# Performance work log

Measured on AMD Instinct MI355X. Metric: run time of the kernel, lower is better.

## Reference

```python
import jax, jax.numpy as jnp
import numpy as np

B, T, E_A, E_B, E_ATT, N_HEAD = 2, 2048, 2048, 2048, 2048, 16
HS = E_ATT // N_HEAD  # 128
ROPE_BASE = 100000.0


def setup_inputs() -> dict:
    key = jax.random.key(0)
    ks = jax.random.split(key, 6)
    Ta = T // 2
    x_a = jax.random.normal(ks[0], (B, Ta, E_A), jnp.float32)
    x_b = jax.random.normal(ks[1], (B, T - Ta, E_B), jnp.float32)
    # alternating text/other tokens: even positions are stream-a
    mask_a = jnp.tile((jnp.arange(T) % 2 == 0)[None, :], (B, 1))
    # standard RoPE tables, full head_size (freqs duplicated), as litgpt/nanoGPT build them
    pos = jnp.arange(T, dtype=jnp.float32)
    inv_freq = 1.0 / (ROPE_BASE ** (jnp.arange(0, HS, 2, dtype=jnp.float32) / HS))
    freqs = pos[:, None] * inv_freq[None, :]           # [T, HS/2]
    emb = jnp.concatenate([freqs, freqs], axis=-1)      # [T, HS]
    cos, sin = jnp.cos(emb), jnp.sin(emb)
    s = 0.02
    Wqkv_a = jax.random.normal(ks[2], (E_A, 3 * E_ATT), jnp.float32) * s
    Wqkv_b = jax.random.normal(ks[3], (E_B, 3 * E_ATT), jnp.float32) * s
    Wproj_a = jax.random.normal(ks[4], (E_ATT, E_A), jnp.float32) * s
    Wproj_b = jax.random.normal(ks[5], (E_ATT, E_B), jnp.float32) * s
    return dict(x_a=x_a, x_b=x_b, cos=cos, sin=sin, mask_a=mask_a,
                Wqkv_a=Wqkv_a, Wqkv_b=Wqkv_b, Wproj_a=Wproj_a, Wproj_b=Wproj_b)


def _apply_rope(x, cos, sin):
    # x: [B, H, T, HS]; cos/sin: [T, HS] broadcast over leading dims
    x1 = x[..., : HS // 2]
    x2 = x[..., HS // 2:]
    rot = jnp.concatenate([-x2, x1], axis=-1)
    return (x * cos + rot * sin).astype(x.dtype)


def reference(x_a, x_b, cos, sin, mask_a, Wqkv_a, Wqkv_b, Wproj_a, Wproj_b):
    Bm, Tm = mask_a.shape
    Na = x_a.shape[0] * x_a.shape[1]  # static token counts per stream
    Nb = x_b.shape[0] * x_b.shape[1]
    C3 = Wqkv_a.shape[1]              # 3 * E_ATT
    # dual-stream QKV projections (bias=False)
    qkv_a = (x_a @ Wqkv_a).reshape(-1, C3)
    qkv_b = (x_b @ Wqkv_b).reshape(-1, C3)
    # interleave tokens back into the full [B, T] layout by mask scatter
    flat = mask_a.reshape(-1)
    idx_a = jnp.nonzero(flat, size=Na)[0]
    idx_b = jnp.nonzero(~flat, size=Nb)[0]
    kqv = jnp.zeros((Bm * Tm, C3), qkv_a.dtype).at[idx_a].set(qkv_a).at[idx_b].set(qkv_b)
    kqv = kqv.reshape(Bm, Tm, 3 * N_HEAD, HS).transpose(0, 2, 1, 3)  # [B, 3H, T, hs]
    q, k, v = kqv[:, :N_HEAD], kqv[:, N_HEAD:2 * N_HEAD], kqv[:, 2 * N_HEAD:]
    q = _apply_rope(q, cos, sin)
    k = _apply_rope(k, cos, sin)
    # causal SDPA (dropout_p = 0 at eval)
    scale = 1.0 / np.sqrt(HS).astype(np.float32)
    att = jnp.einsum('bhqd,bhkd->bhqk', q, k) * scale
    causal = jnp.tril(jnp.ones((Tm, Tm), bool))
    att = jnp.where(causal, att, -jnp.inf)
    att = jax.nn.softmax(att, axis=-1)
    y = jnp.einsum('bhqk,bhkd->bhqd', att, v)
    y = y.transpose(0, 2, 1, 3).reshape(Bm * Tm, N_HEAD * HS)
    # mask split + per-stream output projections
    y_a = y[idx_a] @ Wproj_a
    y_b = y[idx_b] @ Wproj_b
    return (y_a, y_b)
```

## Files before the change

kernel.cpp:

```cpp
#include <hip/hip_runtime.h>
#include <hip/hip_bf16.h>


typedef __attribute__((ext_vector_type(8))) short v8s;
typedef __attribute__((ext_vector_type(4))) float v4f;

#define GL2LDS(gptr, lptr)                                              \
  __builtin_amdgcn_global_load_lds(                                     \
      (const __attribute__((address_space(1))) void*)(gptr),            \
      (__attribute__((address_space(3))) void*)(lptr), 16, 0, 0)

__device__ __forceinline__ float b2f(unsigned short u) {
  return __uint_as_float(((unsigned int)u) << 16);
}
__device__ __forceinline__ unsigned short f2bf(float f) {
  unsigned int u = __float_as_uint(f);
  u += 0x7fffu + ((u >> 16) & 1u);
  return (unsigned short)(u >> 16);
}

__global__ __launch_bounds__(256) void f32_to_bf16_2(
    const float4* __restrict__ a, const float4* __restrict__ b,
    uint2* __restrict__ out, int n4each) {
  int i = blockIdx.x * 256 + threadIdx.x;
  if (i >= 2 * n4each) return;
  float4 v = (i < n4each) ? a[i] : b[i - n4each];
  uint2 o;
  o.x = (unsigned int)f2bf(v.x) | ((unsigned int)f2bf(v.y) << 16);
  o.y = (unsigned int)f2bf(v.z) | ((unsigned int)f2bf(v.w) << 16);
  out[i] = o;
}

__global__ __launch_bounds__(256) void transpose_f32_bf16(
    const float* __restrict__ in0, const float* __restrict__ in1,
    unsigned short* __restrict__ out0, unsigned short* __restrict__ out1,
    int R, int C) {
  const float* in = blockIdx.z ? in1 : in0;
  unsigned short* out = blockIdx.z ? out1 : out0;
  __shared__ unsigned short tile[64][65];
  const int bc = blockIdx.x * 64, br = blockIdx.y * 64;
  const int c  = threadIdx.x & 63;
  const int r0 = threadIdx.x >> 6;
  for (int r = r0; r < 64; r += 4)
    tile[r][c] = f2bf(in[(size_t)(br + r) * C + bc + c]);
  __syncthreads();
  for (int rr = r0; rr < 64; rr += 4)
    out[(size_t)(bc + rr) * R + br + c] = tile[c][rr];
}

template <int MODE>
__device__ __forceinline__ int amap(int r) {
  if constexpr (MODE == 0) return r;
  else return ((r >> 10) << 11) + ((r & 1023) << 1) + (MODE - 1);
}

template <int OMODE>
__global__ __launch_bounds__(256) void gemm_bt(
    const unsigned short* __restrict__ A, const unsigned short* __restrict__ BT,
    unsigned short* __restrict__ C, int M, int N, int K) {
  __shared__ __align__(16) unsigned short As[128 * 32];
  __shared__ __align__(16) unsigned short Bs[128 * 32];
  const int tid = threadIdx.x;
  const int w = tid >> 6, lane = tid & 63;
  const int m0 = blockIdx.x * 128, n0 = blockIdx.y * 128;
  const int wr = (w >> 1) * 64, wc = (w & 1) * 64;
  const int r = lane & 15, q = lane >> 4;

  const int cA  = w * 128 + lane;
  const int row = cA >> 2, kc = cA & 3;
  const unsigned short* gA0 = A  + (size_t)(m0 + row)      * K + kc * 8;
  const unsigned short* gA1 = A  + (size_t)(m0 + row + 16) * K + kc * 8;
  const unsigned short* gB0 = BT + (size_t)(n0 + row)      * K + kc * 8;
  const unsigned short* gB1 = BT + (size_t)(n0 + row + 16) * K + kc * 8;

  v4f acc[4][4] = {};

  for (int k0 = 0; k0 < K; k0 += 32) {
    GL2LDS(gA0 + k0, &As[w * 1024]);
    GL2LDS(gA1 + k0, &As[w * 1024 + 512]);
    GL2LDS(gB0 + k0, &Bs[w * 1024]);
    GL2LDS(gB1 + k0, &Bs[w * 1024 + 512]);
    __builtin_amdgcn_s_waitcnt(0);
    __syncthreads();

    v8s af[4], bf[4];
#pragma unroll
    for (int t = 0; t < 4; ++t) {
      af[t] = *(const v8s*)&As[(wr + t * 16 + r) * 32 + q * 8];
      bf[t] = *(const v8s*)&Bs[(wc + t * 16 + r) * 32 + q * 8];
    }
#pragma unroll
    for (int tm = 0; tm < 4; ++tm)
#pragma unroll
      for (int tn = 0; tn < 4; ++tn)
        acc[tm][tn] = __builtin_amdgcn_mfma_f32_16x16x32_bf16(
            af[tm], bf[tn], acc[tm][tn], 0, 0, 0);
    __builtin_amdgcn_s_waitcnt(0);
    __syncthreads();
  }

#pragma unroll
  for (int tm = 0; tm < 4; ++tm) {
    const int rowm = wr + tm * 16 + q * 4;
#pragma unroll
    for (int tn = 0; tn < 4; ++tn) {
      const int col = n0 + wc + tn * 16 + r;
#pragma unroll
      for (int p = 0; p < 4; ++p) {
        const int orow = amap<OMODE>(m0 + rowm + p);
        C[(size_t)orow * N + col] = f2bf(acc[tm][tn][p]);
      }
    }
  }
}

__global__ __launch_bounds__(256) void gemm_proj(
    const unsigned short* __restrict__ A, const unsigned short* __restrict__ BT0,
    const unsigned short* __restrict__ BT1, float* __restrict__ Cout,
    int M, int N, int K) {
  const int par = blockIdx.z;
  const unsigned short* BT = par ? BT1 : BT0;
  float* C = Cout + (size_t)par * M * N;
  __shared__ __align__(16) unsigned short As[128 * 32];
  __shared__ __align__(16) unsigned short Bs[128 * 32];
  const int tid = threadIdx.x;
  const int w = tid >> 6, lane = tid & 63;
  const int m0 = blockIdx.x * 128, n0 = blockIdx.y * 128;
  const int wr = (w >> 1) * 64, wc = (w & 1) * 64;
  const int r = lane & 15, q = lane >> 4;

  const int cA  = w * 128 + lane;
  const int row = cA >> 2, kc = cA & 3;
  const int ar0 = m0 + row, ar1 = m0 + row + 16;
  const int g0 = ((ar0 >> 10) << 11) + ((ar0 & 1023) << 1) + par;
  const int g1 = ((ar1 >> 10) << 11) + ((ar1 & 1023) << 1) + par;
  const unsigned short* gA0 = A  + (size_t)g0 * K + kc * 8;
  const unsigned short* gA1 = A  + (size_t)g1 * K + kc * 8;
  const unsigned short* gB0 = BT + (size_t)(n0 + row)      * K + kc * 8;
  const unsigned short* gB1 = BT + (size_t)(n0 + row + 16) * K + kc * 8;

  v4f acc[4][4] = {};

  for (int k0 = 0; k0 < K; k0 += 32) {
    GL2LDS(gA0 + k0, &As[w * 1024]);
    GL2LDS(gA1 + k0, &As[w * 1024 + 512]);
    GL2LDS(gB0 + k0, &Bs[w * 1024]);
    GL2LDS(gB1 + k0, &Bs[w * 1024 + 512]);
    __builtin_amdgcn_s_waitcnt(0);
    __syncthreads();

    v8s af[4], bf[4];
#pragma unroll
    for (int t = 0; t < 4; ++t) {
      af[t] = *(const v8s*)&As[(wr + t * 16 + r) * 32 + q * 8];
      bf[t] = *(const v8s*)&Bs[(wc + t * 16 + r) * 32 + q * 8];
    }
#pragma unroll
    for (int tm = 0; tm < 4; ++tm)
#pragma unroll
      for (int tn = 0; tn < 4; ++tn)
        acc[tm][tn] = __builtin_amdgcn_mfma_f32_16x16x32_bf16(
            af[tm], bf[tn], acc[tm][tn], 0, 0, 0);
    __builtin_amdgcn_s_waitcnt(0);
    __syncthreads();
  }

#pragma unroll
  for (int tm = 0; tm < 4; ++tm) {
    const int rowm = m0 + wr + tm * 16 + q * 4;
#pragma unroll
    for (int tn = 0; tn < 4; ++tn) {
      const int col = n0 + wc + tn * 16 + r;
#pragma unroll
      for (int p = 0; p < 4; ++p)
        C[(size_t)(rowm + p) * N + col] = acc[tm][tn][p];
    }
  }
}

__global__ __launch_bounds__(256) void scatter_rope(
    const unsigned short* __restrict__ qkv,
    const float* __restrict__ cosb, const float* __restrict__ sinb,
    unsigned short* __restrict__ Q, unsigned short* __restrict__ K) {
  const int token = blockIdx.x;
  const int b = token >> 11, t = token & 2047;
  const unsigned short* src = qkv + (size_t)token * 6144;
  for (int i = threadIdx.x; i < 2048; i += 256) {
    const int d = i & 127, h = i >> 7;
    const float cv = cosb[t * 128 + d];
    const float sv = sinb[t * 128 + d];
    const int   mate = (d < 64) ? i + 64 : i - 64;
    const float sgn  = (d < 64) ? -1.f : 1.f;
    const float qv = b2f(src[i]),        qm = b2f(src[mate]) * sgn;
    const float kv = b2f(src[2048 + i]), km = b2f(src[2048 + mate]) * sgn;
    const size_t off = ((size_t)(b * 16 + h) * 2048 + t) * 128 + d;
    Q[off] = f2bf(qv * cv + qm * sv);
    K[off] = f2bf(kv * cv + km * sv);
  }
}

__global__ __launch_bounds__(256) void transpose_v(
    const unsigned short* __restrict__ qkv, unsigned short* __restrict__ Vt) {
  __shared__ unsigned short tile[128][129];
  const int bh = blockIdx.x >> 4, tt = blockIdx.x & 15;
  const int b = bh >> 4, h = bh & 15;
  const int tid = threadIdx.x;
  const int d0 = tid & 127, t0 = tid >> 7;
#pragma unroll 4
  for (int i = 0; i < 64; ++i) {
    int tl = i * 2 + t0;
    tile[tl][d0] =
        qkv[((size_t)(b * 2048 + tt * 128 + tl)) * 6144 + 4096 + h * 128 + d0];
  }
  __syncthreads();
#pragma unroll 4
  for (int i = 0; i < 64; ++i) {
    int dd = i * 2 + t0;
    Vt[((size_t)(bh * 128 + dd)) * 2048 + tt * 128 + d0] = tile[d0][dd];
  }
}

#define SIG 0.1275174038536989f

__global__ __launch_bounds__(256, 2) void attn_flash(
    const unsigned short* __restrict__ Q, const unsigned short* __restrict__ K,
    const unsigned short* __restrict__ Vt, unsigned short* __restrict__ Y) {
  __shared__ __align__(16) unsigned short Ks[64 * 128];
  __shared__ __align__(16) unsigned short Vs[128 * 64];
  __shared__ __align__(16) unsigned short QP[64 * 128];

  const int bh = blockIdx.x >> 4, pr = blockIdx.x & 15;
  const int tid = threadIdx.x, w = tid >> 6, lane = tid & 63;
  const int r = lane & 15, q = lane >> 4;
  const int b = bh >> 4, h = bh & 15;
  const size_t kbase = (size_t)bh * 2048 * 128;
  const size_t vbase = (size_t)bh * 128 * 2048;

  for (int ph = 0; ph < 2; ++ph) {
    const int qt = ph ? pr : (31 - pr);

    const size_t qbase = ((size_t)bh * 2048 + qt * 64) * 128;
#pragma unroll
    for (int i = 0; i < 4; ++i) {
      const int rowl = w * 16 + i * 4 + q;
      const int g = r ^ (rowl & 15);
      GL2LDS(Q + qbase + (size_t)rowl * 128 + g * 8, &QP[(w * 16 + i * 4) * 128]);
    }
    __builtin_amdgcn_s_waitcnt(0);
    v8s qf[4];
#pragma unroll
    for (int ki = 0; ki < 4; ++ki) {
      const int rowl = w * 16 + r;
      const int c = (ki * 4 + q) ^ r;
      qf[ki] = *(const v8s*)&QP[rowl * 128 + c * 8];
    }
    __syncthreads();

    float mrun[4], lrun[4];
    v4f O[8] = {};
#pragma unroll
    for (int p = 0; p < 4; ++p) { mrun[p] = -3.0e38f; lrun[p] = 0.f; }

    const int nkt = qt + 1;
    for (int kt = 0; kt < nkt; ++kt) {
#pragma unroll
      for (int i = 0; i < 4; ++i) {
        const int key = w * 16 + i * 4 + q;
        const int g = r ^ (key & 15);
        GL2LDS(K + kbase + ((size_t)kt * 64 + key) * 128 + g * 8,
               &Ks[(w * 16 + i * 4) * 128]);
      }
      const int vrow = lane >> 3, pc = lane & 7;
#pragma unroll
      for (int i = 0; i < 4; ++i) {
        const int d = w * 32 + i * 8 + vrow;
        const int g = pc ^ (d & 7);
        GL2LDS(Vt + vbase + (size_t)d * 2048 + kt * 64 + g * 8,
               &Vs[(w * 32 + i * 8) * 64]);
      }
      __builtin_amdgcn_s_waitcnt(0);
      __syncthreads();

      v4f S[4] = {};
#pragma unroll
      for (int ki = 0; ki < 4; ++ki) {
        v8s kf[4];
#pragma unroll
        for (int tn = 0; tn < 4; ++tn) {
          const int key = tn * 16 + r;
          const int c = (ki * 4 + q) ^ r;
          kf[tn] = *(const v8s*)&Ks[key * 128 + c * 8];
        }
#pragma unroll
        for (int tn = 0; tn < 4; ++tn)
          S[tn] = __builtin_amdgcn_mfma_f32_16x16x32_bf16(
              qf[ki], kf[tn], S[tn], 0, 0, 0);
      }

      if (kt == qt) {
#pragma unroll
        for (int tn = 0; tn < 4; ++tn)
#pragma unroll
          for (int p = 0; p < 4; ++p) {
            const int tq = w * 16 + q * 4 + p;
            const int kg = tn * 16 + r;
            if (kg > tq) S[tn][p] = -3.0e38f;
          }
      }

#pragma unroll
      for (int p = 0; p < 4; ++p) {
        float mx = fmaxf(fmaxf(S[0][p], S[1][p]), fmaxf(S[2][p], S[3][p]));
#pragma unroll
        for (int o = 1; o < 16; o <<= 1) mx = fmaxf(mx, __shfl_xor(mx, o, 64));
        const float mnew = fmaxf(mrun[p], mx);
        const float alpha = exp2f((mrun[p] - mnew) * SIG);
        mrun[p] = mnew;
        float sum = 0.f;
#pragma unroll
        for (int tn = 0; tn < 4; ++tn) {
          const float pv = exp2f((S[tn][p] - mnew) * SIG);
          S[tn][p] = pv;
          sum += pv;
        }
#pragma unroll
        for (int o = 1; o < 16; o <<= 1) sum += __shfl_xor(sum, o, 64);
        lrun[p] = lrun[p] * alpha + sum;
#pragma unroll
        for (int tn = 0; tn < 8; ++tn) O[tn][p] *= alpha;
      }

#pragma unroll
      for (int tn = 0; tn < 4; ++tn)
#pragma unroll
        for (int p = 0; p < 4; ++p) {
          const int m = w * 16 + q * 4 + p;
          QP[m * 72 + tn * 16 + r] = f2bf(S[tn][p]);
        }

#pragma unroll
      for (int ki = 0; ki < 2; ++ki) {
        v8s pf, vf[8];
        const int m = w * 16 + r;
        pf = *(const v8s*)&QP[m * 72 + (ki * 4 + q) * 8];
#pragma unroll
        for (int tn = 0; tn < 8; ++tn) {
          const int d = tn * 16 + r;
          const int c = (ki * 4 + q) ^ (d & 7);
          vf[tn] = *(const v8s*)&Vs[d * 64 + c * 8];
        }
#pragma unroll
        for (int tn = 0; tn < 8; ++tn)
          O[tn] = __builtin_amdgcn_mfma_f32_16x16x32_bf16(
              pf, vf[tn], O[tn], 0, 0, 0);
      }
      __syncthreads();
    }

#pragma unroll
    for (int p = 0; p < 4; ++p) {
      const float inv = 1.0f / lrun[p];
      const int t = qt * 64 + w * 16 + q * 4 + p;
#pragma unroll
      for (int tn = 0; tn < 8; ++tn)
        Y[((size_t)(b * 2048 + t)) * 2048 + h * 128 + tn * 16 + r] =
            f2bf(O[tn][p] * inv);
    }
  }
}

extern "C" void kernel_launch(void* const* d_in, const int* in_sizes, int n_in,
                              void* d_out, int out_size, void* d_ws, size_t ws_size,
                              hipStream_t stream) {
  const float* x_a   = (const float*)d_in[0];
  const float* x_b   = (const float*)d_in[1];
  const float* cosb  = (const float*)d_in[2];
  const float* sinb  = (const float*)d_in[3];
  const float* Wqkv_a  = (const float*)d_in[5];
  const float* Wqkv_b  = (const float*)d_in[6];
  const float* Wproj_a = (const float*)d_in[7];
  const float* Wproj_b = (const float*)d_in[8];
  float* out = (float*)d_out;

  if (ws_size < 100663296u) return;

  char* ws = (char*)d_ws;
  unsigned short* QKVall = (unsigned short*)(ws);
  unsigned short* XA     = (unsigned short*)(ws + 50331648);
  unsigned short* WQT    = (unsigned short*)(ws + 67108864);
  unsigned short* Qb     = (unsigned short*)(ws + 50331648);
  unsigned short* Kb     = (unsigned short*)(ws + 67108864);
  unsigned short* Vtb    = (unsigned short*)(ws + 83886080);
  unsigned short* Yb     = (unsigned short*)(ws);
  unsigned short* WPT_A  = (unsigned short*)(ws + 16777216);
  unsigned short* WPT_B  = (unsigned short*)(ws + 25165824);

  hipLaunchKernelGGL(f32_to_bf16_2, dim3(8192), dim3(256), 0, stream,
                     (const float4*)x_a, (const float4*)x_b, (uint2*)XA, 1048576);
  hipLaunchKernelGGL(transpose_f32_bf16, dim3(96, 32, 1), dim3(256), 0, stream,
                     Wqkv_a, Wqkv_a, WQT, WQT, 2048, 6144);
  hipLaunchKernelGGL((gemm_bt<1>), dim3(16, 48), dim3(256), 0, stream,
                     XA, WQT, QKVall, 2048, 6144, 2048);
  hipLaunchKernelGGL(transpose_f32_bf16, dim3(96, 32, 1), dim3(256), 0, stream,
                     Wqkv_b, Wqkv_b, WQT, WQT, 2048, 6144);
  hipLaunchKernelGGL((gemm_bt<2>), dim3(16, 48), dim3(256), 0, stream,
                     XA + (size_t)4194304, WQT, QKVall, 2048, 6144, 2048);

  hipLaunchKernelGGL(scatter_rope, dim3(4096), dim3(256), 0, stream,
                     QKVall, cosb, sinb, Qb, Kb);
  hipLaunchKernelGGL(transpose_v, dim3(512), dim3(256), 0, stream,
                     QKVall, Vtb);

  hipLaunchKernelGGL(transpose_f32_bf16, dim3(32, 32, 2), dim3(256), 0, stream,
                     Wproj_a, Wproj_b, WPT_A, WPT_B, 2048, 2048);

  hipLaunchKernelGGL(attn_flash, dim3(512), dim3(256), 0, stream,
                     Qb, Kb, Vtb, Yb);

  hipLaunchKernelGGL(gemm_proj, dim3(16, 16, 2), dim3(256), 0, stream,
                     Yb, WPT_A, WPT_B, out, 2048, 2048, 2048);
}
```

Before: 520.7 us.

## Replace GEMMs with pipelined 256x256 tile kernel using swizzled LDS and prefetch

```diff
diff --git a/kernel.cpp b/kernel.cpp
--- a/kernel.cpp
+++ b/kernel.cpp
@@ -9,6 +9,8 @@
   __builtin_amdgcn_global_load_lds(                                     \
       (const __attribute__((address_space(1))) void*)(gptr),            \
       (__attribute__((address_space(3))) void*)(lptr), 16, 0, 0)
+
+#define S_BARRIER() asm volatile("s_barrier" ::: "memory")
 
 __device__ __forceinline__ float b2f(unsigned short u) {
   return __uint_as_float(((unsigned int)u) << 16);
@@ -48,132 +50,171 @@
     out[(size_t)(bc + rr) * R + br + c] = tile[c][rr];
 }
 
-template <int MODE>
-__device__ __forceinline__ int amap(int r) {
-  if constexpr (MODE == 0) return r;
-  else return ((r >> 10) << 11) + ((r & 1023) << 1) + (MODE - 1);
-}
-
-template <int OMODE>
-__global__ __launch_bounds__(256) void gemm_bt(
-    const unsigned short* __restrict__ A, const unsigned short* __restrict__ BT,
-    unsigned short* __restrict__ C, int M, int N, int K) {
-  __shared__ __align__(16) unsigned short As[128 * 32];
-  __shared__ __align__(16) unsigned short Bs[128 * 32];
+template <int MH, int NH>
+__device__ __forceinline__ void mfma_quad(v4f (&acc)[8][4], const v8s (&a)[4][2],
+                                          const v8s (&b)[4][2]) {
+  __builtin_amdgcn_s_setprio(1);
+#pragma unroll
+  for (int ks = 0; ks < 2; ++ks)
+#pragma unroll
+    for (int i = 0; i < 4; ++i)
+#pragma unroll
+      for (int j = 0; j < 2; ++j)
+        acc[MH * 4 + i][NH * 2 + j] = __builtin_amdgcn_mfma_f32_16x16x32_bf16(
+            a[i][ks], b[NH * 2 + j][ks], acc[MH * 4 + i][NH * 2 + j], 0, 0, 0);
+  __builtin_amdgcn_s_setprio(0);
+}
+
+__device__ __forceinline__ void read_a_half(const unsigned short* lds, int base,
+                                            int mh, int r, int c0, int c1,
+                                            v8s (&a)[4][2]) {
+#pragma unroll
+  for (int i = 0; i < 4; ++i) {
+    const unsigned short* ap = lds + base + (mh * 64 + i * 16 + r) * 64;
+    a[i][0] = *(const v8s*)(ap + c0);
+    a[i][1] = *(const v8s*)(ap + c1);
+  }
+}
+
+template <int NH>
+__device__ __forceinline__ void read_b_half(const unsigned short* lds, int base,
+                                            int brow, int r, int c0, int c1,
+                                            v8s (&b)[4][2]) {
+#pragma unroll
+  for (int j = 0; j < 2; ++j) {
+    const unsigned short* bp = lds + base + (brow + (NH * 2 + j) * 16 + r) * 64;
+    b[NH * 2 + j][0] = *(const v8s*)(bp + c0);
+    b[NH * 2 + j][1] = *(const v8s*)(bp + c1);
+  }
+}
+
+template <int GATHER, int OSCAT>
+__global__ __launch_bounds__(512, 2) void gemm256(
+    const unsigned short* __restrict__ A,
+    const unsigned short* __restrict__ BT0,
+    const unsigned short* __restrict__ BT1,
+    void* __restrict__ Cout, int M, int N, int K, int NBN) {
+  __shared__ __align__(16) unsigned short lds[65536];
   const int tid = threadIdx.x;
+  const int par = blockIdx.y;
+  const unsigned short* __restrict__ BT = par ? BT1 : BT0;
+
+  int wg = blockIdx.x;
+  const int cpx = gridDim.x >> 3;
+  wg = (wg & 7) * cpx + (wg >> 3);
+  const int m0 = (wg / NBN) * 256, n0 = (wg % NBN) * 256;
+
   const int w = tid >> 6, lane = tid & 63;
-  const int m0 = blockIdx.x * 128, n0 = blockIdx.y * 128;
-  const int wr = (w >> 1) * 64, wc = (w & 1) * 64;
+  const int wm = w >> 2, wn = w & 3;
   const int r = lane & 15, q = lane >> 4;
-
-  const int cA  = w * 128 + lane;
-  const int row = cA >> 2, kc = cA & 3;
-  const unsigned short* gA0 = A  + (size_t)(m0 + row)      * K + kc * 8;
-  const unsigned short* gA1 = A  + (size_t)(m0 + row + 16) * K + kc * 8;
-  const unsigned short* gB0 = BT + (size_t)(n0 + row)      * K + kc * 8;
-  const unsigned short* gB1 = BT + (size_t)(n0 + row + 16) * K + kc * 8;
-
-  v4f acc[4][4] = {};
-
-  for (int k0 = 0; k0 < K; k0 += 32) {
-    GL2LDS(gA0 + k0, &As[w * 1024]);
-    GL2LDS(gA1 + k0, &As[w * 1024 + 512]);
-    GL2LDS(gB0 + k0, &Bs[w * 1024]);
-    GL2LDS(gB1 + k0, &Bs[w * 1024 + 512]);
-    __builtin_amdgcn_s_waitcnt(0);
-    __syncthreads();
-
-    v8s af[4], bf[4];
-#pragma unroll
-    for (int t = 0; t < 4; ++t) {
-      af[t] = *(const v8s*)&As[(wr + t * 16 + r) * 32 + q * 8];
-      bf[t] = *(const v8s*)&Bs[(wc + t * 16 + r) * 32 + q * 8];
-    }
-#pragma unroll
-    for (int tm = 0; tm < 4; ++tm)
-#pragma unroll
-      for (int tn = 0; tn < 4; ++tn)
-        acc[tm][tn] = __builtin_amdgcn_mfma_f32_16x16x32_bf16(
-            af[tm], bf[tn], acc[tm][tn], 0, 0, 0);
-    __builtin_amdgcn_s_waitcnt(0);
-    __syncthreads();
-  }
-
-#pragma unroll
-  for (int tm = 0; tm < 4; ++tm) {
-    const int rowm = wr + tm * 16 + q * 4;
+  const int rs = r & 7;
+  const int c0 = ((q ^ rs) << 3);
+  const int c1 = (((4 + q) ^ rs) << 3);
+  const int brow = (wn & 1) << 6;
+  const int AbaseE = (2 + wm) * 8192, BbaseE = (wn >> 1) * 8192;
+  const int AbaseO = (6 + wm) * 8192, BbaseO = (4 + (wn >> 1)) * 8192;
+
+  const int sr0 = tid >> 3, sslot = tid & 7;
+  const int NT = K >> 6, NIT = NT >> 1;
+
+  auto stageB = [&](int p, int tt) {
+    unsigned short* dst = &lds[(((tt << 2) + p) & 7) * 8192 + w * 512];
+#pragma unroll
+    for (int cc = 0; cc < 2; ++cc) {
+      const int row = sr0 + cc * 64;
+      const int g = ((sslot ^ (row & 7)) << 3);
+      GL2LDS(BT + (size_t)(n0 + p * 128 + row) * K + tt * 64 + g, dst + cc * 4096);
+    }
+  };
+  auto stageA = [&](int p, int tt) {
+    unsigned short* dst = &lds[(((tt << 2) + 2 + p) & 7) * 8192 + w * 512];
+#pragma unroll
+    for (int cc = 0; cc < 2; ++cc) {
+      const int row = sr0 + cc * 64;
+      const int g = ((sslot ^ (row & 7)) << 3);
+      int ar = m0 + p * 128 + row;
+      if constexpr (GATHER) ar = ((ar >> 10) << 11) + ((ar & 1023) << 1) + par;
+      GL2LDS(A + (size_t)ar * K + tt * 64 + g, dst + cc * 4096);
+    }
+  };
+
+  v4f acc[8][4] = {};
+  v8s a[4][2], b[4][2];
+
+  stageB(0, 0); stageB(1, 0); stageA(0, 0); stageA(1, 0);
+  asm volatile("" ::: "memory");
+  stageB(0, 1); stageB(1, 1);
+  asm volatile("s_waitcnt vmcnt(4)" ::: "memory");
+  S_BARRIER();
+
+  for (int it = 0; it < NIT; ++it) {
+    const int t = it << 1;
+    const bool more = (it + 1 < NIT);
+
+    read_a_half(lds, AbaseE, 0, r, c0, c1, a);
+    read_b_half<0>(lds, BbaseE, brow, r, c0, c1, b);
+    stageA(0, t + 1);
+    S_BARRIER();
+    mfma_quad<0, 0>(acc, a, b);
+    S_BARRIER();
+    read_b_half<1>(lds, BbaseE, brow, r, c0, c1, b);
+    stageA(1, t + 1);
+    S_BARRIER();
+    mfma_quad<0, 1>(acc, a, b);
+    S_BARRIER();
+    read_a_half(lds, AbaseE, 1, r, c0, c1, a);
+    if (more) stageB(0, t + 2);
+    S_BARRIER();
+    mfma_quad<1, 0>(acc, a, b);
+    S_BARRIER();
+    if (more) stageB(1, t + 2);
+    S_BARRIER();
+    mfma_quad<1, 1>(acc, a, b);
+    if (more) { asm volatile("s_waitcnt vmcnt(4)" ::: "memory"); }
+    else      { asm volatile("s_waitcnt vmcnt(0)" ::: "memory"); }
+    S_BARRIER();
+
+    read_a_half(lds, AbaseO, 0, r, c0, c1, a);
+    read_b_half<0>(lds, BbaseO, brow, r, c0, c1, b);
+    if (more) stageA(0, t + 2);
+    S_BARRIER();
+    mfma_quad<0, 0>(acc, a, b);
+    S_BARRIER();
+    read_b_half<1>(lds, BbaseO, brow, r, c0, c1, b);
+    if (more) stageA(1, t + 2);
+    S_BARRIER();
+    mfma_quad<0, 1>(acc, a, b);
+    S_BARRIER();
+    read_a_half(lds, AbaseO, 1, r, c0, c1, a);
+    if (more) stageB(0, t + 3);
+    S_BARRIER();
+    mfma_quad<1, 0>(acc, a, b);
+    S_BARRIER();
+    if (more) stageB(1, t + 3);
+    S_BARRIER();
+    mfma_quad<1, 1>(acc, a, b);
+    if (more) { asm volatile("s_waitcnt vmcnt(4)" ::: "memory"); }
+    S_BARRIER();
+  }
+
+  float* Cf = (float*)Cout + (size_t)par * M * N;
+  unsigned short* Cb = (unsigned short*)Cout;
+#pragma unroll
+  for (int tm = 0; tm < 8; ++tm) {
+    const int rowm = m0 + wm * 128 + tm * 16 + q * 4;
 #pragma unroll
     for (int tn = 0; tn < 4; ++tn) {
-      const int col = n0 + wc + tn * 16 + r;
+      const int col = n0 + wn * 64 + tn * 16 + r;
 #pragma unroll
       for (int p = 0; p < 4; ++p) {
-        const int orow = amap<OMODE>(m0 + rowm + p);
-        C[(size_t)orow * N + col] = f2bf(acc[tm][tn][p]);
-      }
-    }
-  }
-}
-
-__global__ __launch_bounds__(256) void gemm_proj(
-    const unsigned short* __restrict__ A, const unsigned short* __restrict__ BT0,
-    const unsigned short* __restrict__ BT1, float* __restrict__ Cout,
-    int M, int N, int K) {
-  const int par = blockIdx.z;
-  const unsigned short* BT = par ? BT1 : BT0;
-  float* C = Cout + (size_t)par * M * N;
-  __shared__ __align__(16) unsigned short As[128 * 32];
-  __shared__ __align__(16) unsigned short Bs[128 * 32];
-  const int tid = threadIdx.x;
-  const int w = tid >> 6, lane = tid & 63;
-  const int m0 = blockIdx.x * 128, n0 = blockIdx.y * 128;
-  const int wr = (w >> 1) * 64, wc = (w & 1) * 64;
-  const int r = lane & 15, q = lane >> 4;
-
-  const int cA  = w * 128 + lane;
-  const int row = cA >> 2, kc = cA & 3;
-  const int ar0 = m0 + row, ar1 = m0 + row + 16;
-  const int g0 = ((ar0 >> 10) << 11) + ((ar0 & 1023) << 1) + par;
-  const int g1 = ((ar1 >> 10) << 11) + ((ar1 & 1023) << 1) + par;
-  const unsigned short* gA0 = A  + (size_t)g0 * K + kc * 8;
-  const unsigned short* gA1 = A  + (size_t)g1 * K + kc * 8;
-  const unsigned short* gB0 = BT + (size_t)(n0 + row)      * K + kc * 8;
-  const unsigned short* gB1 = BT + (size_t)(n0 + row + 16) * K + kc * 8;
-
-  v4f acc[4][4] = {};
-
-  for (int k0 = 0; k0 < K; k0 += 32) {
-    GL2LDS(gA0 + k0, &As[w * 1024]);
-    GL2LDS(gA1 + k0, &As[w * 1024 + 512]);
-    GL2LDS(gB0 + k0, &Bs[w * 1024]);
-    GL2LDS(gB1 + k0, &Bs[w * 1024 + 512]);
-    __builtin_amdgcn_s_waitcnt(0);
-    __syncthreads();
-
-    v8s af[4], bf[4];
-#pragma unroll
-    for (int t = 0; t < 4; ++t) {
-      af[t] = *(const v8s*)&As[(wr + t * 16 + r) * 32 + q * 8];
-      bf[t] = *(const v8s*)&Bs[(wc + t * 16 + r) * 32 + q * 8];
-    }
-#pragma unroll
-    for (int tm = 0; tm < 4; ++tm)
-#pragma unroll
-      for (int tn = 0; tn < 4; ++tn)
-        acc[tm][tn] = __builtin_amdgcn_mfma_f32_16x16x32_bf16(
-            af[tm], bf[tn], acc[tm][tn], 0, 0, 0);
-    __builtin_amdgcn_s_waitcnt(0);
-    __syncthreads();
-  }
-
-#pragma unroll
-  for (int tm = 0; tm < 4; ++tm) {
-    const int rowm = m0 + wr + tm * 16 + q * 4;
-#pragma unroll
-    for (int tn = 0; tn < 4; ++tn) {
-      const int col = n0 + wc + tn * 16 + r;
-#pragma unroll
-      for (int p = 0; p < 4; ++p)
-        C[(size_t)(rowm + p) * N + col] = acc[tm][tn][p];
+        if constexpr (OSCAT == 0) {
+          Cf[(size_t)(rowm + p) * N + col] = acc[tm][tn][p];
+        } else {
+          const int ar = rowm + p;
+          const int orow = ((ar >> 10) << 11) + ((ar & 1023) << 1) + (OSCAT - 1);
+          Cb[(size_t)orow * N + col] = f2bf(acc[tm][tn][p]);
+        }
+      }
     }
   }
 }
@@ -399,12 +440,12 @@
                      (const float4*)x_a, (const float4*)x_b, (uint2*)XA, 1048576);
   hipLaunchKernelGGL(transpose_f32_bf16, dim3(96, 32, 1), dim3(256), 0, stream,
                      Wqkv_a, Wqkv_a, WQT, WQT, 2048, 6144);
-  hipLaunchKernelGGL((gemm_bt<1>), dim3(16, 48), dim3(256), 0, stream,
-                     XA, WQT, QKVall, 2048, 6144, 2048);
+  hipLaunchKernelGGL((gemm256<0, 1>), dim3(192, 1), dim3(512), 0, stream,
+                     XA, WQT, WQT, QKVall, 2048, 6144, 2048, 24);
   hipLaunchKernelGGL(transpose_f32_bf16, dim3(96, 32, 1), dim3(256), 0, stream,
                      Wqkv_b, Wqkv_b, WQT, WQT, 2048, 6144);
-  hipLaunchKernelGGL((gemm_bt<2>), dim3(16, 48), dim3(256), 0, stream,
-                     XA + (size_t)4194304, WQT, QKVall, 2048, 6144, 2048);
+  hipLaunchKernelGGL((gemm256<0, 2>), dim3(192, 1), dim3(512), 0, stream,
+                     XA + (size_t)4194304, WQT, WQT, QKVall, 2048, 6144, 2048, 24);
 
   hipLaunchKernelGGL(scatter_rope, dim3(4096), dim3(256), 0, stream,
                      QKVall, cosb, sinb, Qb, Kb);
@@ -417,6 +458,6 @@
   hipLaunchKernelGGL(attn_flash, dim3(512), dim3(256), 0, stream,
                      Qb, Kb, Vtb, Yb);
 
-  hipLaunchKernelGGL(gemm_proj, dim3(16, 16, 2), dim3(256), 0, stream,
-                     Yb, WPT_A, WPT_B, out, 2048, 2048, 2048);
-}
+  hipLaunchKernelGGL((gemm256<1, 0>), dim3(64, 2), dim3(512), 0, stream,
+                     Yb, WPT_A, WPT_B, out, 2048, 2048, 2048, 8);
+}
```

Result: faster. 497.8 us (-4.4%).
